# Kernel optimization log

Measured on AMD Instinct MI355X. Metric: run time of the kernel, lower is better.

The kernel has to match this reference:

```python
import jax, jax.numpy as jnp
import numpy as np


def _conv_bn_relu(x, w, g, b):
    # 1x1 conv over channel dim + BatchNorm(eval, affine) + ReLU; x: [B,Cin,...]
    y = jnp.einsum('oc,bc...->bo...', w, x)
    shp = (1, -1) + (1,) * (y.ndim - 2)
    return jax.nn.relu(y * g.reshape(shp) + b.reshape(shp))


def _gather(feat, idx):
    # feat [B,d,N], idx [B,M] -> [B,d,M]  (torch.gather along dim 2)
    return jnp.take_along_axis(feat, idx[:, None, :], axis=2)


def _lfa(f, neigh_idx, w, g, b):
    # Local Feature Aggregation: gather k neighbors, concat with center, 1x1 conv, max over k.
    Bn, Np, k = neigh_idx.shape
    fs = f[..., 0]                                   # [B,d,N]
    d = fs.shape[1]
    neigh = _gather(fs, neigh_idx.reshape(Bn, Np * k)).reshape(Bn, d, Np, k)
    cat = jnp.concatenate([jnp.broadcast_to(f, neigh.shape), neigh], axis=1)  # [B,2d,N,k]
    return _conv_bn_relu(cat, w, g, b).max(axis=3, keepdims=True)             # [B,d_out,N,1]


def _random_sample(f, pool_idx):
    # f [B,d,N,1], pool_idx [B,N',k] -> [B,d,N',1] via gather + max over k
    Bn, Np, k = pool_idx.shape
    fs = f[..., 0]
    d = fs.shape[1]
    gth = _gather(fs, pool_idx.reshape(Bn, Np * k)).reshape(Bn, d, Np, k)
    return gth.max(axis=3, keepdims=True)


def _interp(f, interp_idx):
    # f [B,d,N,1], interp_idx [B,M,1] -> [B,d,M,1] nearest-neighbor upsample
    Bn, M, _ = interp_idx.shape
    return _gather(f[..., 0], interp_idx.reshape(Bn, M))[..., None]


def setup_inputs() -> dict:
    key = jax.random.key(0)
    B, K = 2, 16
    Ns = (16384, 4096, 1024, 256, 64)
    ks = list(jax.random.split(key, 64))
    ki = iter(ks)
    inp = {}
    inp['xyz'] = jax.random.normal(next(ki), (B, Ns[0], 3), jnp.float32)
    for i in range(4):
        inp['neigh%d' % i] = jax.random.randint(next(ki), (B, Ns[i], K), 0, Ns[i], jnp.int32)
        inp['pool%d' % i] = jax.random.randint(next(ki), (B, Ns[i + 1], K), 0, Ns[i], jnp.int32)
        inp['up%d' % i] = jax.random.randint(next(ki), (B, Ns[i], 1), 0, Ns[i + 1], jnp.int32)

    def mk(name, co, cin):
        inp[name + '_w'] = jax.random.normal(next(ki), (co, cin), jnp.float32) * 0.02
        inp[name + '_g'] = jnp.ones((co,), jnp.float32)
        inp[name + '_b'] = jnp.zeros((co,), jnp.float32)

    mk('fc0', 64, 3)
    mk('l1', 128, 128)
    mk('l2', 256, 256)
    mk('l3', 512, 512)
    mk('l4', 1024, 1024)
    mk('dt', 1024, 1024)
    mk('d4', 512, 2048)
    mk('d3', 256, 1024)
    mk('d2', 128, 512)
    mk('d1', 64, 256)
    mk('d0', 64, 64)
    return inp


def reference(xyz, neigh0, neigh1, neigh2, neigh3, pool0, pool1, pool2, pool3, up0, up1, up2, up3, fc0_w, fc0_g, fc0_b, l1_w, l1_g, l1_b, l2_w, l2_g, l2_b, l3_w, l3_g, l3_b, l4_w, l4_g, l4_b, dt_w, dt_g, dt_b, d4_w, d4_g, d4_b, d3_w, d3_g, d3_b, d2_w, d2_g, d2_b, d1_w, d1_g, d1_b, d0_w, d0_g, d0_b):
    out0 = _conv_bn_relu(jnp.transpose(xyz, (0, 2, 1)), fc0_w, fc0_g, fc0_b)[..., None]  # [B,64,N0,1]
    out1 = _lfa(out0, neigh0, l1_w, l1_g, l1_b)        # [B,128,N0,1]
    out1p = _random_sample(out1, pool0)                # [B,128,N1,1]
    out2 = _lfa(out1p, neigh1, l2_w, l2_g, l2_b)       # [B,256,N1,1]
    out2p = _random_sample(out2, pool1)                # [B,256,N2,1]
    out3 = _lfa(out2p, neigh2, l3_w, l3_g, l3_b)       # [B,512,N2,1]
    out3p = _random_sample(out3, pool2)                # [B,512,N3,1]
    out4 = _lfa(out3p, neigh3, l4_w, l4_g, l4_b)       # [B,1024,N3,1]
    out4p = _random_sample(out4, pool3)                # [B,1024,N4,1]
    out = _conv_bn_relu(out4p, dt_w, dt_g, dt_b)
    out = _conv_bn_relu(jnp.concatenate([out, out4p], 1), d4_w, d4_g, d4_b)
    out = _interp(out, up3)
    out = _conv_bn_relu(jnp.concatenate([out, out3p], 1), d3_w, d3_g, d3_b)
    out = _interp(out, up2)
    out = _conv_bn_relu(jnp.concatenate([out, out2p], 1), d2_w, d2_g, d2_b)
    out = _interp(out, up1)
    out = _conv_bn_relu(jnp.concatenate([out, out1p], 1), d1_w, d1_g, d1_b)
    out = _interp(out, up0)
    out = _conv_bn_relu(out, d0_w, d0_g, d0_b)         # [B,out_d,N0,1]
    return out
```

## Files before the change

kernel.cpp:

```cpp
#include <hip/hip_runtime.h>

typedef unsigned short u16;
typedef unsigned int u32;
typedef short s16x8 __attribute__((ext_vector_type(8)));
typedef float f32x4 __attribute__((ext_vector_type(4)));

__device__ __forceinline__ float bf2f(u16 u) {
  union { u32 i; float f; } c;
  c.i = ((u32)u) << 16;
  return c.f;
}
__device__ __forceinline__ u16 f2bf(float f) {
  union { float f; u32 i; } c;
  c.f = f;
  u32 r = c.i + 0x7FFFu + ((c.i >> 16) & 1u);
  return (u16)(r >> 16);
}
__device__ __forceinline__ float rbf(float x) {
  union { float f; u32 u; } c;
  c.f = x;
  u32 r = c.u + 0x7FFFu + ((c.u >> 16) & 1u);
  c.u = (r >> 16) << 16;
  return c.f;
}
__device__ __forceinline__ float ldin(const void* p, size_t i, int isBf) {
  if (isBf) return bf2f(((const u16*)p)[i]);
  return rbf(((const float*)p)[i]);
}
__device__ __forceinline__ void ld4bf(const u16* p, float* v) {
  uint2 q = *reinterpret_cast<const uint2*>(p);
  v[0] = bf2f((u16)(q.x & 0xFFFFu));
  v[1] = bf2f((u16)(q.x >> 16));
  v[2] = bf2f((u16)(q.y & 0xFFFFu));
  v[3] = bf2f((u16)(q.y >> 16));
}
__device__ __forceinline__ void st4bf(u16* p, const float* v) {
  uint2 q;
  q.x = (u32)f2bf(v[0]) | (((u32)f2bf(v[1])) << 16);
  q.y = (u32)f2bf(v[2]) | (((u32)f2bf(v[3])) << 16);
  *reinterpret_cast<uint2*>(p) = q;
}

__global__ void C3Dnet_34600256537193_kernel() {}

__global__ void probe_kernel(const u16* x, int* flag) {
  if (threadIdx.x == 0 && blockIdx.x == 0) {
    int sane = 0;
    for (int i = 0; i < 256; i += 2) {
      int e = (x[i] >> 7) & 0xFF;
      if (e >= 97 && e <= 137) ++sane;
    }
    *flag = (sane >= 64) ? 1 : 0;
  }
}

__global__ __launch_bounds__(256) void sentinel_kernel(u16* out, int n, float v) {
  u16 u = f2bf(v);
  int i0 = (blockIdx.x * 256 + threadIdx.x) * 8;
  for (int j = 0; j < 8; ++j)
    if (i0 + j < n) out[i0 + j] = u;
}

__global__ __launch_bounds__(256) void cvt_kernel(
    const void* s0, const void* s1, const void* s2, const void* s3, const void* s4,
    const void* s5, const void* s6, const void* s7, const void* s8, const void* s9,
    u16* dst, const int* dtF) {
  const int f = *dtF;
  int blk = blockIdx.x;
  const void* src;
  int base, boff;
  if (blk < 8)         { src = s0; base = 0;       boff = 0;    }
  else if (blk < 40)   { src = s1; base = 16384;   boff = 8;    }
  else if (blk < 168)  { src = s2; base = 81920;   boff = 40;   }
  else if (blk < 680)  { src = s3; base = 344064;  boff = 168;  }
  else if (blk < 1192) { src = s4; base = 1392640; boff = 680;  }
  else if (blk < 1704) { src = s5; base = 2441216; boff = 1192; }
  else if (blk < 1832) { src = s6; base = 3489792; boff = 1704; }
  else if (blk < 1864) { src = s7; base = 3751936; boff = 1832; }
  else if (blk < 1872) { src = s8; base = 3817472; boff = 1864; }
  else                 { src = s9; base = 3833856; boff = 1872; }
  int local = (blk - boff) * 2048 + (int)threadIdx.x * 8;
  u16* dp = dst + base + local;
  if (f) {
    *reinterpret_cast<uint4*>(dp) =
        *reinterpret_cast<const uint4*>((const u16*)src + local);
  } else {
    const float4* sp = reinterpret_cast<const float4*>((const float*)src + local);
    float4 a = sp[0], b = sp[1];
    uint4 o;
    o.x = (u32)f2bf(a.x) | (((u32)f2bf(a.y)) << 16);
    o.y = (u32)f2bf(a.z) | (((u32)f2bf(a.w)) << 16);
    o.z = (u32)f2bf(b.x) | (((u32)f2bf(b.y)) << 16);
    o.w = (u32)f2bf(b.z) | (((u32)f2bf(b.w)) << 16);
    *reinterpret_cast<uint4*>(dp) = o;
  }
}

__global__ __launch_bounds__(256) void fc0_kernel(
    const void* xyz, const void* w, const void* g, const void* be,
    u16* out, int N, const int* dtF) {
  int f = *dtF;
  int o = threadIdx.x & 63;
  int n = blockIdx.x * 4 + (threadIdx.x >> 6);
  int b = blockIdx.y;
  if (n >= N) return;
  size_t pb = ((size_t)b * N + n) * 3;
  float acc = ldin(w, o * 3 + 0, f) * ldin(xyz, pb + 0, f) +
              ldin(w, o * 3 + 1, f) * ldin(xyz, pb + 1, f) +
              ldin(w, o * 3 + 2, f) * ldin(xyz, pb + 2, f);
  acc = acc * ldin(g, o, f) + ldin(be, o, f);
  if (acc < 0.0f) acc = 0.0f;
  out[((size_t)b * N + n) * 64 + o] = f2bf(acc);
}

__global__ __launch_bounds__(256) void gather_max_kernel(
    const void* src, int srcBf16, int srcStride, int srcOff, int Nsrc,
    const void* cen, int cenBf16, int cenStride,
    const int* idx, void* out, int outBf16, int Np, int C, int doRelu) {
  int c4n = C >> 2;
  int ptsPerBlk = 256 / c4n;
  int p = (int)threadIdx.x / c4n;
  int c4 = (int)threadIdx.x % c4n;
  int n = blockIdx.x * ptsPerBlk + p;
  int b = blockIdx.y;
  if (n >= Np) return;
  const int* ip = idx + ((size_t)b * Np + n) * 16;
  float m[4];
  m[0] = m[1] = m[2] = m[3] = -3.0e38f;
  for (int k = 0; k < 16; ++k) {
    size_t base = ((size_t)b * Nsrc + ip[k]) * srcStride + srcOff + (c4 << 2);
    float v[4];
    if (srcBf16) {
      ld4bf((const u16*)src + base, v);
    } else {
      float4 t = *reinterpret_cast<const float4*>((const float*)src + base);
      v[0] = t.x; v[1] = t.y; v[2] = t.z; v[3] = t.w;
    }
    for (int j = 0; j < 4; ++j)
      if (v[j] > m[j]) m[j] = v[j];
  }
  if (cen) {
    size_t cb = ((size_t)b * Np + n) * cenStride + (c4 << 2);
    float cv[4];
    if (cenBf16) {
      ld4bf((const u16*)cen + cb, cv);
    } else {
      float4 t = *reinterpret_cast<const float4*>((const float*)cen + cb);
      cv[0] = t.x; cv[1] = t.y; cv[2] = t.z; cv[3] = t.w;
    }
    for (int j = 0; j < 4; ++j) m[j] += cv[j];
  }
  if (doRelu) {
    for (int j = 0; j < 4; ++j)
      if (m[j] < 0.0f) m[j] = 0.0f;
  }
  size_t ob = ((size_t)b * Np + n) * C + (c4 << 2);
  if (outBf16) {
    st4bf((u16*)out + ob, m);
  } else {
    float4 t;
    t.x = m[0]; t.y = m[1]; t.z = m[2]; t.w = m[3];
    *reinterpret_cast<float4*>((float*)out + ob) = t;
  }
}

__global__ __launch_bounds__(256) void mfma_gemm_kernel(
    const u16* W, int wld,
    const u16* X, int cin, int Nn,
    const void* gamma, const void* beta,
    void* out, int outBf16,
    int OD, int odHalf, int doRelu, const int* dtF) {
  __shared__ u16 Ws[128 * 40];
  const int f = *dtF;
  const int b = blockIdx.z;
  const int n0 = blockIdx.x * 64;
  const int o0 = blockIdx.y * 128;
  const int tid = threadIdx.x;
  const int wid = tid >> 6;
  const int lane = tid & 63;
  const int lr = lane & 15;
  const int lq = lane >> 4;

  f32x4 acc0 = {0.f,0.f,0.f,0.f}, acc1 = acc0, acc2 = acc0, acc3 = acc0;
  f32x4 acc4 = acc0, acc5 = acc0, acc6 = acc0, acc7 = acc0;

  const u16* xp = X + ((size_t)b * Nn + (n0 + wid * 16 + lr)) * cin + lq * 8;

  for (int kk = 0; kk < cin; kk += 32) {
    for (int i = 0; i < 2; ++i) {
      int idx = tid + i * 256;
      int row = idx >> 2, q = idx & 3;
      int o = o0 + row;
      int wr = o, ko = 0;
      if (odHalf && o >= odHalf) { wr = o - odHalf; ko = cin; }
      *reinterpret_cast<uint4*>(&Ws[row * 40 + q * 8]) =
          *reinterpret_cast<const uint4*>(W + (size_t)wr * wld + ko + kk + q * 8);
    }
    __syncthreads();
    s16x8 a = *reinterpret_cast<const s16x8*>(xp + kk);
    s16x8 b0 = *reinterpret_cast<const s16x8*>(&Ws[(0 * 16 + lr) * 40 + lq * 8]);
    acc0 = __builtin_amdgcn_mfma_f32_16x16x32_bf16(a, b0, acc0, 0, 0, 0);
    s16x8 b1 = *reinterpret_cast<const s16x8*>(&Ws[(1 * 16 + lr) * 40 + lq * 8]);
    acc1 = __builtin_amdgcn_mfma_f32_16x16x32_bf16(a, b1, acc1, 0, 0, 0);
    s16x8 b2 = *reinterpret_cast<const s16x8*>(&Ws[(2 * 16 + lr) * 40 + lq * 8]);
    acc2 = __builtin_amdgcn_mfma_f32_16x16x32_bf16(a, b2, acc2, 0, 0, 0);
    s16x8 b3 = *reinterpret_cast<const s16x8*>(&Ws[(3 * 16 + lr) * 40 + lq * 8]);
    acc3 = __builtin_amdgcn_mfma_f32_16x16x32_bf16(a, b3, acc3, 0, 0, 0);
    s16x8 b4 = *reinterpret_cast<const s16x8*>(&Ws[(4 * 16 + lr) * 40 + lq * 8]);
    acc4 = __builtin_amdgcn_mfma_f32_16x16x32_bf16(a, b4, acc4, 0, 0, 0);
    s16x8 b5 = *reinterpret_cast<const s16x8*>(&Ws[(5 * 16 + lr) * 40 + lq * 8]);
    acc5 = __builtin_amdgcn_mfma_f32_16x16x32_bf16(a, b5, acc5, 0, 0, 0);
    s16x8 b6 = *reinterpret_cast<const s16x8*>(&Ws[(6 * 16 + lr) * 40 + lq * 8]);
    acc6 = __builtin_amdgcn_mfma_f32_16x16x32_bf16(a, b6, acc6, 0, 0, 0);
    s16x8 b7 = *reinterpret_cast<const s16x8*>(&Ws[(7 * 16 + lr) * 40 + lq * 8]);
    acc7 = __builtin_amdgcn_mfma_f32_16x16x32_bf16(a, b7, acc7, 0, 0, 0);
    __syncthreads();
  }

  f32x4 av[8] = {acc0, acc1, acc2, acc3, acc4, acc5, acc6, acc7};
  #pragma unroll
  for (int ot = 0; ot < 8; ++ot) {
    int o = o0 + ot * 16 + lr;
    int og = (odHalf && o >= odHalf) ? (o - odHalf) : o;
    float ga = ldin(gamma, og, f);
    float bb = (!odHalf || o < odHalf) ? ldin(beta, og, f) : 0.0f;
    #pragma unroll
    for (int r = 0; r < 4; ++r) {
      int n = n0 + wid * 16 + lq * 4 + r;
      float x = av[ot][r] * ga + bb;
      if (doRelu && x < 0.0f) x = 0.0f;
      size_t oi = ((size_t)b * Nn + n) * OD + o;
      if (outBf16) ((u16*)out)[oi] = f2bf(x);
      else ((float*)out)[oi] = x;
    }
  }
}

#define DEF_SGEMV(KNAME, P)                                                        \
__global__ __launch_bounds__(256) void KNAME(                                      \
    const u16* Wc, const void* Wraw, int useCvt, int wld,                          \
    const float* X1, int cin1, int n1src,                                          \
    const float* X2, int cin2, int x2bf,                                           \
    const int* map1,                                                               \
    const void* gamma, const void* beta,                                           \
    float* out,                                                                    \
    int N, int OD, int odHalf, int doRelu, const int* dtF, int nf4Log) {           \
  extern __shared__ float xrow[];                                                  \
  const int f = *dtF;                                                              \
  const int b = blockIdx.y;                                                        \
  const int odt = OD >> 6;                                                         \
  const int ng = (int)blockIdx.x / odt;                                            \
  const int o0 = ((int)blockIdx.x % odt) * 64;                                     \
  const int n0 = ng * P;                                                           \
  const int nf4 = 1 << nf4Log;                                                     \
  const int cin = nf4 << 2;                                                        \
  const int tid = threadIdx.x;                                                     \
  for (int idx4 = tid; idx4 < (P * cin) >> 2; idx4 += 256) {                       \
    int p = idx4 >> nf4Log;                                                        \
    int c = (idx4 & (nf4 - 1)) << 2;                                               \
    int n = n0 + p;                                                                \
    float v4[4];                                                                   \
    if (c < cin1) {                                                                \
      int rs = map1 ? map1[(size_t)b * N + n] : n;                                 \
      float4 v = *reinterpret_cast<const float4*>(X1 + ((size_t)b * n1src + rs) * cin1 + c); \
      v4[0] = v.x; v4[1] = v.y; v4[2] = v.z; v4[3] = v.w;                          \
    } else {                                                                       \
      size_t xo = ((size_t)b * N + n) * cin2 + (c - cin1);                         \
      if (x2bf) {                                                                  \
        ld4bf((const u16*)(const void*)X2 + xo, v4);                               \
      } else {                                                                     \
        float4 v = *reinterpret_cast<const float4*>(X2 + xo);                      \
        v4[0] = v.x; v4[1] = v.y; v4[2] = v.z; v4[3] = v.w;                        \
      }                                                                            \
    }                                                                              \
    xrow[(p << (nf4Log + 2)) + c + 0] = v4[0];                                     \
    xrow[(p << (nf4Log + 2)) + c + 1] = v4[1];                                     \
    xrow[(p << (nf4Log + 2)) + c + 2] = v4[2];                                     \
    xrow[(p << (nf4Log + 2)) + c + 3] = v4[3];                                     \
  }                                                                                \
  __syncthreads();                                                                 \
  const int o = o0 + (tid >> 2);                                                   \
  const int q = tid & 3;                                                           \
  int wr = o, wo = 0, useBeta = 1;                                                 \
  if (odHalf && o >= odHalf) { wr = o - odHalf; wo = cin1; useBeta = 0; }          \
  float sums[P];                                                                   \
  _Pragma("unroll") for (int p = 0; p < P; ++p) sums[p] = 0.0f;                    \
  if (useCvt) {                                                                    \
    const u16* wp = Wc + (size_t)wr * wld + wo;                                    \
    for (int i = q; i < nf4; i += 4) {                                             \
      float wv[4];                                                                 \
      ld4bf(wp + (i << 2), wv);                                                    \
      _Pragma("unroll") for (int p = 0; p < P; ++p) {                              \
        const float4 xv = *reinterpret_cast<const float4*>(                        \
            &xrow[(p << (nf4Log + 2)) + (i << 2)]);                                \
        sums[p] += wv[0] * xv.x + wv[1] * xv.y + wv[2] * xv.z + wv[3] * xv.w;      \
      }                                                                            \
    }                                                                              \
  } else if (f) {                                                                  \
    const u16* wp = (const u16*)Wraw + (size_t)wr * wld + wo;                      \
    for (int i = q; i < nf4; i += 4) {                                             \
      float wv[4];                                                                 \
      ld4bf(wp + (i << 2), wv);                                                    \
      _Pragma("unroll") for (int p = 0; p < P; ++p) {                              \
        const float4 xv = *reinterpret_cast<const float4*>(                        \
            &xrow[(p << (nf4Log + 2)) + (i << 2)]);                                \
        sums[p] += wv[0] * xv.x + wv[1] * xv.y + wv[2] * xv.z + wv[3] * xv.w;      \
      }                                                                            \
    }                                                                              \
  } else {                                                                         \
    const float* wp = (const float*)Wraw + (size_t)wr * wld + wo;                  \
    for (int i = q; i < nf4; i += 4) {                                             \
      float4 wv = *reinterpret_cast<const float4*>(wp + (i << 2));                 \
      float w0 = rbf(wv.x), w1 = rbf(wv.y), w2 = rbf(wv.z), w3 = rbf(wv.w);        \
      _Pragma("unroll") for (int p = 0; p < P; ++p) {                              \
        const float4 xv = *reinterpret_cast<const float4*>(                        \
            &xrow[(p << (nf4Log + 2)) + (i << 2)]);                                \
        sums[p] += w0 * xv.x + w1 * xv.y + w2 * xv.z + w3 * xv.w;                  \
      }                                                                            \
    }                                                                              \
  }                                                                                \
  _Pragma("unroll") for (int p = 0; p < P; ++p) {                                  \
    sums[p] += __shfl_xor(sums[p], 1);                                             \
    sums[p] += __shfl_xor(sums[p], 2);                                             \
  }                                                                                \
  int og = (odHalf && o >= odHalf) ? (o - odHalf) : o;                             \
  float ga = ldin(gamma, og, f);                                                   \
  float bb = useBeta ? ldin(beta, og, f) : 0.0f;                                   \
  _Pragma("unroll") for (int pp = 0; pp < P / 4; ++pp) {                           \
    int p = q * (P / 4) + pp;                                                      \
    float x = sums[p] * ga + bb;                                                   \
    if (doRelu && x < 0.0f) x = 0.0f;                                              \
    out[((size_t)b * N + (n0 + p)) * OD + o] = x;                                  \
  }                                                                                \
}

DEF_SGEMV(sgemv_p4, 4)
DEF_SGEMV(sgemv_p8, 8)
DEF_SGEMV(sgemv_p16, 16)

#define GTK 16
#define LSTR 68
__global__ __launch_bounds__(256) void gemm_kernel(
    const u16* Wc, const void* Wraw, int useCvt, int wld,
    const void* X1, int x1bf16, int cin1, int n1src,
    const float* X2, int cin2,
    const int* map1,
    const void* gamma, const void* beta,
    void* out, int outMode,
    int N, int OD, int odHalf, int doRelu, const int* dtF) {
  __shared__ float XsT[GTK * LSTR];
  __shared__ float WsT[GTK * LSTR];
  const int f = *dtF;
  const int b = blockIdx.z;
  const int n0 = blockIdx.x * 64;
  const int o0 = blockIdx.y * 64;
  const int tid = threadIdx.x;
  const int tx = tid & 15;
  const int ty = tid >> 4;
  const int cin = cin1 + cin2;
  float acc[4][4];
  for (int i = 0; i < 4; ++i)
    for (int j = 0; j < 4; ++j) acc[i][j] = 0.0f;

  for (int kk = 0; kk < cin; kk += GTK) {
    for (int l = 0; l < 4; ++l) {
      int e = tid + l * 256;
      int r = e >> 4, c = e & 15;
      int cc = kk + c;
      int n = n0 + r;
      float v = 0.0f;
      if (cc < cin) {
        if (cc < cin1) {
          int rs = map1 ? map1[(size_t)b * N + n] : n;
          size_t xi = ((size_t)b * n1src + rs) * cin1 + cc;
          v = x1bf16 ? bf2f(((const u16*)X1)[xi]) : ((const float*)X1)[xi];
        } else {
          v = X2[((size_t)b * N + n) * cin2 + (cc - cin1)];
        }
      }
      XsT[c * LSTR + r] = v;
    }
    for (int l = 0; l < 4; ++l) {
      int e = tid + l * 256;
      int r = e >> 4, c = e & 15;
      int o = o0 + r, cc = kk + c;
      float v = 0.0f;
      if (cc < cin) {
        int wr = o, wo = 0;
        if (odHalf && o >= odHalf) { wr = o - odHalf; wo = cin1; }
        size_t wi = (size_t)wr * wld + wo + cc;
        v = useCvt ? bf2f(Wc[wi]) : ldin(Wraw, wi, f);
      }
      WsT[c * LSTR + r] = v;
    }
    __syncthreads();
    #pragma unroll
    for (int c = 0; c < GTK; ++c) {
      float a4[4], w4[4];
      *reinterpret_cast<float4*>(a4) =
          *reinterpret_cast<const float4*>(&XsT[c * LSTR + ty * 4]);
      *reinterpret_cast<float4*>(w4) =
          *reinterpret_cast<const float4*>(&WsT[c * LSTR + tx * 4]);
      for (int i = 0; i < 4; ++i)
        for (int j = 0; j < 4; ++j) acc[i][j] += a4[i] * w4[j];
    }
    __syncthreads();
  }

  if (outMode == 2) {
    for (int j = 0; j < 4; ++j) {
      int o = o0 + tx * 4 + j;
      float ga = ldin(gamma, o, f), bb = ldin(beta, o, f);
      float x4[4];
      for (int i = 0; i < 4; ++i) {
        float x = acc[i][j] * ga + bb;
        if (doRelu && x < 0.0f) x = 0.0f;
        x4[i] = x;
      }
      size_t po = ((size_t)b * OD + o) * N + n0 + ty * 4;
      if (f) {
        uint2 q;
        q.x = (u32)f2bf(x4[0]) | (((u32)f2bf(x4[1])) << 16);
        q.y = (u32)f2bf(x4[2]) | (((u32)f2bf(x4[3])) << 16);
        *reinterpret_cast<uint2*>((u16*)out + po) = q;
      } else {
        float4 t;
        t.x = x4[0]; t.y = x4[1]; t.z = x4[2]; t.w = x4[3];
        *reinterpret_cast<float4*>((float*)out + po) = t;
      }
    }
  } else {
    for (int i = 0; i < 4; ++i) {
      int n = n0 + ty * 4 + i;
      float vv[4];
      for (int j = 0; j < 4; ++j) {
        int o = o0 + tx * 4 + j;
        float x = acc[i][j];
        int og = (odHalf && o >= odHalf) ? (o - odHalf) : o;
        x *= ldin(gamma, og, f);
        if (!odHalf || o < odHalf) x += ldin(beta, og, f);
        if (doRelu && x < 0.0f) x = 0.0f;
        vv[j] = x;
      }
      size_t ob = ((size_t)b * N + n) * OD + o0 + tx * 4;
      if (outMode == 1) {
        st4bf((u16*)out + ob, vv);
      } else {
        float4 t;
        t.x = vv[0]; t.y = vv[1]; t.z = vv[2]; t.w = vv[3];
        *reinterpret_cast<float4*>((float*)out + ob) = t;
      }
    }
  }
}

extern "C" void kernel_launch(void* const* d_in, const int* in_sizes, int n_in,
                              void* d_out, int out_size, void* d_ws, size_t ws_size,
                              hipStream_t stream) {
  (void)in_sizes;
  (void)n_in;
  const int B = 2;
  const int N0 = 16384, N1 = 4096, N2 = 1024, N3 = 256, N4 = 64;
  const int* nb0 = (const int*)d_in[1];
  const int* pl0 = (const int*)d_in[2];
  const int* up0 = (const int*)d_in[3];
  const int* nb1 = (const int*)d_in[4];
  const int* pl1 = (const int*)d_in[5];
  const int* up1 = (const int*)d_in[6];
  const int* nb2 = (const int*)d_in[7];
  const int* pl2 = (const int*)d_in[8];
  const int* up2 = (const int*)d_in[9];
  const int* nb3 = (const int*)d_in[10];
  const int* pl3 = (const int*)d_in[11];
  const int* up3 = (const int*)d_in[12];

  {
    float v = 1000.0f + 4.0f * (float)(ws_size >> 20);
    int nblk = (out_size + 2047) / 2048;
    sentinel_kernel<<<dim3(nblk), dim3(256), 0, stream>>>((u16*)d_out, out_size, v);
  }

  float* ws = (float*)d_ws;
  u16* out1p = (u16*)(ws + 0);
  u16* out2p = (u16*)(ws + 1048576);
  float* out3p = ws + 1572864;
  float* out4p = ws + 1835008;
  const size_t TZ = 1966080;
  u16* cpgp1 = (u16*)(ws + TZ);
  u16* out0 = (u16*)(ws + TZ + 4194304);
  u16* out1 = (u16*)(ws + TZ + 4194304);
  u16* cpgp2 = (u16*)(ws + TZ);
  float* out2 = ws + TZ + 2097152;
  float* cpgp3 = ws + TZ;
  float* out3 = ws + TZ + 2097152;
  float* cpgp4 = ws + TZ;
  float* out4 = ws + TZ + 1048576;
  float* dto = ws + TZ;
  float* d4o = ws + TZ + 131072;
  float* d3o = ws + TZ + 196608;
  float* d2o = ws + TZ + 327680;
  float* d1o = ws + TZ + 589824;
  int* dtF = (int*)(ws + TZ + 6291456);
  u16* wcvt = (u16*)(ws + TZ + 6291456 + 8);

  const size_t NEED_MIN = (TZ + 6291456 + 4) * sizeof(float);
  const size_t NEED_BIG = (TZ + 6291456 + 8 + 1918976) * sizeof(float);
  if (d_ws == 0 || ws_size < NEED_MIN) return;
  const int CVT = (ws_size >= NEED_BIG) ? 1 : 0;

  u16* w_l1 = wcvt + 0;
  u16* w_l2 = wcvt + 16384;
  u16* w_l3 = wcvt + 81920;
  u16* w_l4 = wcvt + 344064;
  u16* w_dt = wcvt + 1392640;
  u16* w_d4 = wcvt + 2441216;
  u16* w_d3 = wcvt + 3489792;
  u16* w_d2 = wcvt + 3751936;
  u16* w_d1 = wcvt + 3817472;
  u16* w_d0 = wcvt + 3833856;

  probe_kernel<<<dim3(1), dim3(64), 0, stream>>>((const u16*)d_in[0], dtF);
  if (CVT) {
    cvt_kernel<<<dim3(1874), dim3(256), 0, stream>>>(
        d_in[16], d_in[19], d_in[22], d_in[25], d_in[28],
        d_in[31], d_in[34], d_in[37], d_in[40], d_in[43], wcvt, dtF);
  }

  fc0_kernel<<<dim3(N0 / 4, B), dim3(256), 0, stream>>>(
      d_in[0], d_in[13], d_in[14], d_in[15], out0, N0, dtF);

  if (CVT) {
    mfma_gemm_kernel<<<dim3(N0 / 64, 256 / 128, B), dim3(256), 0, stream>>>(
        w_l1, 128, out0, 64, N0, d_in[17], d_in[18], cpgp1, 1, 256, 128, 0, dtF);
  } else {
    gemm_kernel<<<dim3(N0 / 64, 256 / 64, B), dim3(256), 0, stream>>>(
        w_l1, d_in[16], CVT, 128, out0, 1, 64, N0, (const float*)0, 0, (const int*)0,
        d_in[17], d_in[18], cpgp1, 1, N0, 256, 128, 0, dtF);
  }
  gather_max_kernel<<<dim3(N0 / 8, B), dim3(256), 0, stream>>>(
      cpgp1, 1, 256, 128, N0, cpgp1, 1, 256, nb0, out1, 1, N0, 128, 1);
  gather_max_kernel<<<dim3(N1 / 8, B), dim3(256), 0, stream>>>(
      out1, 1, 128, 0, N0, (const void*)0, 0, 0, pl0, out1p, 1, N1, 128, 0);

  if (CVT) {
    mfma_gemm_kernel<<<dim3(N1 / 64, 512 / 128, B), dim3(256), 0, stream>>>(
        w_l2, 256, out1p, 128, N1, d_in[20], d_in[21], cpgp2, 1, 512, 256, 0, dtF);
  } else {
    gemm_kernel<<<dim3(N1 / 64, 512 / 64, B), dim3(256), 0, stream>>>(
        w_l2, d_in[19], CVT, 256, out1p, 1, 128, N1, (const float*)0, 0, (const int*)0,
        d_in[20], d_in[21], cpgp2, 1, N1, 512, 256, 0, dtF);
  }
  gather_max_kernel<<<dim3(N1 / 4, B), dim3(256), 0, stream>>>(
      cpgp2, 1, 512, 256, N1, cpgp2, 1, 512, nb1, out2, 0, N1, 256, 1);
  gather_max_kernel<<<dim3(N2 / 4, B), dim3(256), 0, stream>>>(
      out2, 0, 256, 0, N1, (const void*)0, 0, 0, pl1, out2p, 1, N2, 256, 0);

  if (CVT) {
    mfma_gemm_kernel<<<dim3(N2 / 64, 1024 / 128, B), dim3(256), 0, stream>>>(
        w_l3, 512, out2p, 256, N2, d_in[23], d_in[24], cpgp3, 0, 1024, 512, 0, dtF);
  } else {
    gemm_kernel<<<dim3(N2 / 64, 1024 / 64, B), dim3(256), 0, stream>>>(
        w_l3, d_in[22], CVT, 512, out2p, 1, 256, N2, (const float*)0, 0, (const int*)0,
        d_in[23], d_in[24], cpgp3, 0, N2, 1024, 512, 0, dtF);
  }
  gather_max_kernel<<<dim3(N2 / 2, B), dim3(256), 0, stream>>>(
      cpgp3, 0, 1024, 512, N2, cpgp3, 0, 1024, nb2, out3, 0, N2, 512, 1);
  gather_max_kernel<<<dim3(N3 / 2, B), dim3(256), 0, stream>>>(
      out3, 0, 512, 0, N2, (const void*)0, 0, 0, pl2, out3p, 0, N3, 512, 0);

  sgemv_p16<<<dim3((N3 / 16) * (2048 / 64), B), dim3(256), 32768, stream>>>(
      w_l4, d_in[25], CVT, 1024, out3p, 512, N3, (const float*)0, 0, 0, (const int*)0,
      d_in[26], d_in[27], cpgp4, N3, 2048, 1024, 0, dtF, 7);
  gather_max_kernel<<<dim3(N3, B), dim3(256), 0, stream>>>(
      cpgp4, 0, 2048, 1024, N3, cpgp4, 0, 2048, nb3, out4, 0, N3, 1024, 1);
  gather_max_kernel<<<dim3(N4, B), dim3(256), 0, stream>>>(
      out4, 0, 1024, 0, N3, (const void*)0, 0, 0, pl3, out4p, 0, N4, 1024, 0);

  sgemv_p8<<<dim3((N4 / 8) * (1024 / 64), B), dim3(256), 32768, stream>>>(
      w_dt, d_in[28], CVT, 1024, out4p, 1024, N4, (const float*)0, 0, 0, (const int*)0,
      d_in[29], d_in[30], dto, N4, 1024, 0, 1, dtF, 8);
  sgemv_p4<<<dim3((N4 / 4) * (512 / 64), B), dim3(256), 32768, stream>>>(
      w_d4, d_in[31], CVT, 2048, dto, 1024, N4, out4p, 1024, 0, (const int*)0,
      d_in[32], d_in[33], d4o, N4, 512, 0, 1, dtF, 9);
  sgemv_p8<<<dim3((N3 / 8) * (256 / 64), B), dim3(256), 32768, stream>>>(
      w_d3, d_in[34], CVT, 1024, d4o, 512, N4, out3p, 512, 0, up3,
      d_in[35], d_in[36], d3o, N3, 256, 0, 1, dtF, 8);
  sgemv_p16<<<dim3((N2 / 16) * (128 / 64), B), dim3(256), 32768, stream>>>(
      w_d2, d_in[37], CVT, 512, d3o, 256, N3, (const float*)(void*)out2p, 256, 1, up2,
      d_in[38], d_in[39], d2o, N2, 128, 0, 1, dtF, 7);
  sgemv_p16<<<dim3((N1 / 16) * (64 / 64), B), dim3(256), 16384, stream>>>(
      w_d1, d_in[40], CVT, 256, d2o, 128, N2, (const float*)(void*)out1p, 128, 1, up1,
      d_in[41], d_in[42], d1o, N1, 64, 0, 1, dtF, 6);
  gemm_kernel<<<dim3(N0 / 64, 64 / 64, B), dim3(256), 0, stream>>>(
      w_d0, d_in[43], CVT, 64, d1o, 0, 64, N1, (const float*)0, 0, up0,
      d_in[44], d_in[45], d_out, 2, N0, 64, 0, 1, dtF);
}
```

Baseline: 331.7 us.

## Add 8-wide bf16 gather-max kernel and route layer-4 conv through MFMA GEMM

Adds a gather_max8 kernel that loads 8 bf16 channels per 16-byte access and uses it for the bf16-source neighbor and pool gathers in layers 1 and 2. The layer-3 pool output is now stored as bf16 when CVT is set, so the layer-4 1x1 conv can use the MFMA GEMM instead of the fp32 sgemv, and the d3 decoder reads that skip input as bf16. The aim is fewer memory transactions in the gathers and tensor-core throughput for layer 4. In exchange the skip tensor loses precision to bf16 and the dtype flags must stay consistent between producer and consumers.

Measured after the change: 302.7 us. 1.1x faster.

```diff
diff --git a/kernel.cpp b/kernel.cpp
--- a/kernel.cpp
+++ b/kernel.cpp
@@ -161,6 +161,63 @@
     float4 t;
     t.x = m[0]; t.y = m[1]; t.z = m[2]; t.w = m[3];
     *reinterpret_cast<float4*>((float*)out + ob) = t;
+  }
+}
+
+__global__ __launch_bounds__(256) void gather_max8_kernel(
+    const u16* src, int srcStride, int srcOff, int Nsrc,
+    const u16* cen, int cenStride,
+    const int* idx, void* out, int outBf16, int Np, int C, int doRelu) {
+  int c8n = C >> 3;
+  int ptsPerBlk = 256 / c8n;
+  int p = (int)threadIdx.x / c8n;
+  int c8 = (int)threadIdx.x % c8n;
+  int n = blockIdx.x * ptsPerBlk + p;
+  int b = blockIdx.y;
+  if (n >= Np) return;
+  const int* ip = idx + ((size_t)b * Np + n) * 16;
+  float m[8];
+  #pragma unroll
+  for (int j = 0; j < 8; ++j) m[j] = -3.0e38f;
+  for (int k = 0; k < 16; ++k) {
+    const u16* sp = src + ((size_t)b * Nsrc + ip[k]) * srcStride + srcOff + (c8 << 3);
+    uint4 q = *reinterpret_cast<const uint4*>(sp);
+    float v[8];
+    v[0] = bf2f((u16)(q.x & 0xFFFFu)); v[1] = bf2f((u16)(q.x >> 16));
+    v[2] = bf2f((u16)(q.y & 0xFFFFu)); v[3] = bf2f((u16)(q.y >> 16));
+    v[4] = bf2f((u16)(q.z & 0xFFFFu)); v[5] = bf2f((u16)(q.z >> 16));
+    v[6] = bf2f((u16)(q.w & 0xFFFFu)); v[7] = bf2f((u16)(q.w >> 16));
+    #pragma unroll
+    for (int j = 0; j < 8; ++j)
+      if (v[j] > m[j]) m[j] = v[j];
+  }
+  if (cen) {
+    const u16* cp = cen + ((size_t)b * Np + n) * cenStride + (c8 << 3);
+    uint4 q = *reinterpret_cast<const uint4*>(cp);
+    m[0] += bf2f((u16)(q.x & 0xFFFFu)); m[1] += bf2f((u16)(q.x >> 16));
+    m[2] += bf2f((u16)(q.y & 0xFFFFu)); m[3] += bf2f((u16)(q.y >> 16));
+    m[4] += bf2f((u16)(q.z & 0xFFFFu)); m[5] += bf2f((u16)(q.z >> 16));
+    m[6] += bf2f((u16)(q.w & 0xFFFFu)); m[7] += bf2f((u16)(q.w >> 16));
+  }
+  if (doRelu) {
+    #pragma unroll
+    for (int j = 0; j < 8; ++j)
+      if (m[j] < 0.0f) m[j] = 0.0f;
+  }
+  size_t ob = ((size_t)b * Np + n) * C + (c8 << 3);
+  if (outBf16) {
+    uint4 q;
+    q.x = (u32)f2bf(m[0]) | (((u32)f2bf(m[1])) << 16);
+    q.y = (u32)f2bf(m[2]) | (((u32)f2bf(m[3])) << 16);
+    q.z = (u32)f2bf(m[4]) | (((u32)f2bf(m[5])) << 16);
+    q.w = (u32)f2bf(m[6]) | (((u32)f2bf(m[7])) << 16);
+    *reinterpret_cast<uint4*>((u16*)out + ob) = q;
+  } else {
+    float4 t0, t1;
+    t0.x = m[0]; t0.y = m[1]; t0.z = m[2]; t0.w = m[3];
+    t1.x = m[4]; t1.y = m[5]; t1.z = m[6]; t1.w = m[7];
+    *reinterpret_cast<float4*>((float*)out + ob) = t0;
+    *reinterpret_cast<float4*>((float*)out + ob + 4) = t1;
   }
 }
 
@@ -537,10 +594,10 @@
         w_l1, d_in[16], CVT, 128, out0, 1, 64, N0, (const float*)0, 0, (const int*)0,
         d_in[17], d_in[18], cpgp1, 1, N0, 256, 128, 0, dtF);
   }
-  gather_max_kernel<<<dim3(N0 / 8, B), dim3(256), 0, stream>>>(
-      cpgp1, 1, 256, 128, N0, cpgp1, 1, 256, nb0, out1, 1, N0, 128, 1);
-  gather_max_kernel<<<dim3(N1 / 8, B), dim3(256), 0, stream>>>(
-      out1, 1, 128, 0, N0, (const void*)0, 0, 0, pl0, out1p, 1, N1, 128, 0);
+  gather_max8_kernel<<<dim3(N0 / 16, B), dim3(256), 0, stream>>>(
+      cpgp1, 256, 128, N0, cpgp1, 256, nb0, out1, 1, N0, 128, 1);
+  gather_max8_kernel<<<dim3(N1 / 16, B), dim3(256), 0, stream>>>(
+      out1, 128, 0, N0, (const u16*)0, 0, pl0, out1p, 1, N1, 128, 0);
 
   if (CVT) {
     mfma_gemm_kernel<<<dim3(N1 / 64, 512 / 128, B), dim3(256), 0, stream>>>(
@@ -550,8 +607,8 @@
         w_l2, d_in[19], CVT, 256, out1p, 1, 128, N1, (const float*)0, 0, (const int*)0,
         d_in[20], d_in[21], cpgp2, 1, N1, 512, 256, 0, dtF);
   }
-  gather_max_kernel<<<dim3(N1 / 4, B), dim3(256), 0, stream>>>(
-      cpgp2, 1, 512, 256, N1, cpgp2, 1, 512, nb1, out2, 0, N1, 256, 1);
+  gather_max8_kernel<<<dim3(N1 / 8, B), dim3(256), 0, stream>>>(
+      cpgp2, 512, 256, N1, cpgp2, 512, nb1, out2, 0, N1, 256, 1);
   gather_max_kernel<<<dim3(N2 / 4, B), dim3(256), 0, stream>>>(
       out2, 0, 256, 0, N1, (const void*)0, 0, 0, pl1, out2p, 1, N2, 256, 0);
 
@@ -566,11 +623,17 @@
   gather_max_kernel<<<dim3(N2 / 2, B), dim3(256), 0, stream>>>(
       cpgp3, 0, 1024, 512, N2, cpgp3, 0, 1024, nb2, out3, 0, N2, 512, 1);
   gather_max_kernel<<<dim3(N3 / 2, B), dim3(256), 0, stream>>>(
-      out3, 0, 512, 0, N2, (const void*)0, 0, 0, pl2, out3p, 0, N3, 512, 0);
-
-  sgemv_p16<<<dim3((N3 / 16) * (2048 / 64), B), dim3(256), 32768, stream>>>(
-      w_l4, d_in[25], CVT, 1024, out3p, 512, N3, (const float*)0, 0, 0, (const int*)0,
-      d_in[26], d_in[27], cpgp4, N3, 2048, 1024, 0, dtF, 7);
+      out3, 0, 512, 0, N2, (const void*)0, 0, 0, pl2, out3p, CVT, N3, 512, 0);
+
+  if (CVT) {
+    mfma_gemm_kernel<<<dim3(N3 / 64, 2048 / 128, B), dim3(256), 0, stream>>>(
+        w_l4, 1024, (const u16*)(void*)out3p, 512, N3, d_in[26], d_in[27],
+        cpgp4, 0, 2048, 1024, 0, dtF);
+  } else {
+    sgemv_p16<<<dim3((N3 / 16) * (2048 / 64), B), dim3(256), 32768, stream>>>(
+        w_l4, d_in[25], CVT, 1024, out3p, 512, N3, (const float*)0, 0, 0, (const int*)0,
+        d_in[26], d_in[27], cpgp4, N3, 2048, 1024, 0, dtF, 7);
+  }
   gather_max_kernel<<<dim3(N3, B), dim3(256), 0, stream>>>(
       cpgp4, 0, 2048, 1024, N3, cpgp4, 0, 2048, nb3, out4, 0, N3, 1024, 1);
   gather_max_kernel<<<dim3(N4, B), dim3(256), 0, stream>>>(
@@ -583,7 +646,7 @@
       w_d4, d_in[31], CVT, 2048, dto, 1024, N4, out4p, 1024, 0, (const int*)0,
       d_in[32], d_in[33], d4o, N4, 512, 0, 1, dtF, 9);
   sgemv_p8<<<dim3((N3 / 8) * (256 / 64), B), dim3(256), 32768, stream>>>(
-      w_d3, d_in[34], CVT, 1024, d4o, 512, N4, out3p, 512, 0, up3,
+      w_d3, d_in[34], CVT, 1024, d4o, 512, N4, out3p, 512, CVT, up3,
       d_in[35], d_in[36], d3o, N3, 256, 0, 1, dtF, 8);
   sgemv_p16<<<dim3((N2 / 16) * (128 / 64), B), dim3(256), 32768, stream>>>(
       w_d2, d_in[37], CVT, 512, d3o, 256, N3, (const float*)(void*)out2p, 256, 1, up2,
```
